# Kernel optimization log

Measured on AMD Instinct MI355X. Metric: run time of the kernel, lower is better.

## Reference

```python
import jax, jax.numpy as jnp
import numpy as np

D_MODEL = 2048
N_HEAD = 16
B, T = 2, 2048
D_HEAD = D_MODEL // N_HEAD          # 128
D_Q = D_MODEL // 3                  # 682
D_KV = D_MODEL // 2                 # 1024
D_QK_N = D_HEAD // 2                # 64
D_QK_R = D_HEAD // 2                # 64
LN_EPS = 1e-5


def setup_inputs() -> dict:
    key = jax.random.key(0)
    ks = jax.random.split(key, 8)
    s = 0.02
    return {
        'x': jax.random.normal(ks[0], (B, T, D_MODEL), dtype=jnp.float32),
        'Wdq_w': jax.random.normal(ks[1], (D_Q, D_MODEL), dtype=jnp.float32) * s,
        'Wdq_b': jnp.zeros((D_Q,), jnp.float32),
        'qn_g': jnp.ones((D_Q,), jnp.float32),
        'qn_b': jnp.zeros((D_Q,), jnp.float32),
        'Wuq_w': jax.random.normal(ks[2], (D_MODEL, D_Q), dtype=jnp.float32) * s,
        'Wuq_b': jnp.zeros((D_MODEL,), jnp.float32),
        'Wdkv_w': jax.random.normal(ks[3], (D_KV + D_QK_R, D_MODEL), dtype=jnp.float32) * s,
        'Wdkv_b': jnp.zeros((D_KV + D_QK_R,), jnp.float32),
        'kvn_g': jnp.ones((D_KV,), jnp.float32),
        'kvn_b': jnp.zeros((D_KV,), jnp.float32),
        'Wukv_w': jax.random.normal(ks[4], (D_MODEL + N_HEAD * D_QK_N, D_KV), dtype=jnp.float32) * s,
        'Wukv_b': jnp.zeros((D_MODEL + N_HEAD * D_QK_N,), jnp.float32),
        'Wo_w': jax.random.normal(ks[5], (D_MODEL, D_MODEL), dtype=jnp.float32) * s,
        'Wo_b': jnp.zeros((D_MODEL,), jnp.float32),
    }


def _linear(x, w, b):
    return jnp.einsum('...i,oi->...o', x, w) + b


def _layernorm(x, g, b):
    mu = jnp.mean(x, axis=-1, keepdims=True)
    var = jnp.mean(jnp.square(x - mu), axis=-1, keepdims=True)
    return (x - mu) * jax.lax.rsqrt(var + LN_EPS) * g + b


def _rotary(x):
    # Faithful to source: positions are taken from axis 1 of x (B, A, T, d)
    A, d = x.shape[1], x.shape[-1]
    inv_freq = (1.0 / 10000.0) ** (jnp.arange(0, d, 2, dtype=jnp.float32) / d)
    freqs = jnp.arange(A, dtype=jnp.float32)[:, None] * inv_freq[None, :]
    cos = jnp.cos(freqs)[None, :, None, :]
    sin = jnp.sin(freqs)[None, :, None, :]
    x1, x2 = jnp.split(x, 2, axis=-1)
    return jnp.concatenate([x1 * cos + x2 * sin, -x1 * sin + x2 * cos], axis=-1)


def reference(x, Wdq_w, Wdq_b, qn_g, qn_b, Wuq_w, Wuq_b,
              Wdkv_w, Wdkv_b, kvn_g, kvn_b, Wukv_w, Wukv_b, Wo_w, Wo_b):
    Bx, Tx, C = x.shape
    # Q path: down-proj -> norm -> up-proj
    c_q = _layernorm(_linear(x, Wdq_w, Wdq_b), qn_g, qn_b)
    q = _linear(c_q, Wuq_w, Wuq_b).reshape(Bx, Tx, N_HEAD, D_HEAD).transpose(0, 2, 1, 3)
    q_n, q_r = q[..., :D_QK_N], q[..., D_QK_N:]
    q_r = _rotary(q_r)
    # KV path
    c_kv = _linear(x, Wdkv_w, Wdkv_b)
    kv_n, k_r = c_kv[..., :D_KV], c_kv[..., D_KV:]
    kv_n = _layernorm(kv_n, kvn_g, kvn_b)
    kv = _linear(kv_n, Wukv_w, Wukv_b).reshape(Bx, Tx, N_HEAD, D_HEAD + D_QK_N).transpose(0, 2, 1, 3)
    k_n, v = kv[..., :D_QK_N], kv[..., D_QK_N:]
    k_r = k_r.reshape(Bx, Tx, 1, D_QK_R).transpose(0, 2, 1, 3)  # (B,1,T,dr)
    k_r = _rotary(k_r)  # identity here (single position), kept for fidelity
    k_r = jnp.broadcast_to(k_r, (Bx, N_HEAD, Tx, D_QK_R))
    q_full = jnp.concatenate([q_n, q_r], axis=-1)   # (B,H,T,d_head)
    k_full = jnp.concatenate([k_n, k_r], axis=-1)   # (B,H,T,d_head)
    # causal SDPA (scale = 1/sqrt(q dim))
    scale = 1.0 / np.sqrt(D_HEAD)
    scores = jnp.einsum('bhqd,bhkd->bhqk', q_full, k_full) * scale
    causal = jnp.tril(jnp.ones((Tx, Tx), dtype=bool))
    scores = jnp.where(causal[None, None], scores, jnp.finfo(scores.dtype).min)
    p = jax.nn.softmax(scores, axis=-1)
    y = jnp.einsum('bhqk,bhkd->bhqd', p, v)
    y = y.transpose(0, 2, 1, 3).reshape(Bx, Tx, C)
    return _linear(y, Wo_w, Wo_b)
```

## Files before the change

kernel.cpp:

```cpp
#include <hip/hip_runtime.h>
#include <math.h>

#define TOK 4096
#define DM 2048
#define DQ 682
#define DQP 704
#define DKV 1024
#define DUKV 3072
#define NH 16
#define T_SEQ 2048
#define NQKV 1792

typedef __attribute__((ext_vector_type(8))) short short8;
typedef __attribute__((ext_vector_type(4))) float floatx4;
typedef __attribute__((ext_vector_type(2))) unsigned int uint2v;

__device__ __forceinline__ unsigned short f2bf(float f) {
  union { float f; unsigned int u; } v; v.f = f;
  unsigned int u = v.u;
  u += 0x7fffu + ((u >> 16) & 1u);
  return (unsigned short)(u >> 16);
}
__device__ __forceinline__ unsigned short f2bf_fast(float f) {
  union { float f; unsigned int u; } v; v.f = f;
  return (unsigned short)((v.u + 0x8000u) >> 16);
}

typedef __attribute__((address_space(1))) const unsigned int as1_u32;
typedef __attribute__((address_space(3))) unsigned int as3_u32;
__device__ __forceinline__ void async16(const void* g, void* l) {
  __builtin_amdgcn_global_load_lds((as1_u32*)g, (as3_u32*)l, 16, 0, 0);
}

__global__ __launch_bounds__(256) void gemm_dqkv_sk(
    const unsigned short* __restrict__ A,
    const unsigned short* __restrict__ B,
    float* __restrict__ P0, float* __restrict__ P1)
{
  __shared__ __align__(16) unsigned short sm[16384];
  const int kz = blockIdx.z;
  const unsigned short* Ab = A + kz * 1024;
  const unsigned short* Bb = B + kz * 1024;
  float* C = kz ? P1 : P0;
  const int K = 1024;

  const int tid = threadIdx.x;
  const int w = tid >> 6, lane = tid & 63, q = lane >> 4, r = lane & 15;
  const int bm = blockIdx.y * 128, bn = blockIdx.x * 128;

  floatx4 acc[4][4];
#pragma unroll
  for (int i = 0; i < 4; i++)
#pragma unroll
    for (int j = 0; j < 4; j++) acc[i][j] = (floatx4){0.f, 0.f, 0.f, 0.f};

  const int srow = tid >> 2, scol = (tid & 3) * 8;
  const unsigned short* Ag0 = Ab + (size_t)(bm + srow) * 2048 + scol;
  const unsigned short* Ag1 = Ab + (size_t)(bm + 64 + srow) * 2048 + scol;
  const unsigned short* Bg0 = Bb + (size_t)(bn + srow) * 2048 + scol;
  const unsigned short* Bg1 = Bb + (size_t)(bn + 64 + srow) * 2048 + scol;
  const int mrow0 = (w >> 1) * 64, ncol0 = (w & 1) * 64;

  async16(Ag0, &sm[w * 512]);
  async16(Ag1, &sm[2048 + w * 512]);
  async16(Bg0, &sm[8192 + w * 512]);
  async16(Bg1, &sm[8192 + 2048 + w * 512]);

  for (int k0 = 0; k0 < K; k0 += 32) {
    const int cur = (k0 >> 5) & 1;
    __syncthreads();
    if (k0 + 32 < K) {
      const int nxt = cur ^ 1;
      async16(Ag0 + k0 + 32, &sm[nxt * 4096 + w * 512]);
      async16(Ag1 + k0 + 32, &sm[nxt * 4096 + 2048 + w * 512]);
      async16(Bg0 + k0 + 32, &sm[8192 + nxt * 4096 + w * 512]);
      async16(Bg1 + k0 + 32, &sm[8192 + nxt * 4096 + 2048 + w * 512]);
    }
    const unsigned short* As = &sm[cur * 4096];
    const unsigned short* Bs = &sm[8192 + cur * 4096];
    short8 a[4], b[4];
#pragma unroll
    for (int i = 0; i < 4; i++)
      a[i] = *(const short8*)&As[(mrow0 + i * 16 + r) * 32 + q * 8];
#pragma unroll
    for (int j = 0; j < 4; j++)
      b[j] = *(const short8*)&Bs[(ncol0 + j * 16 + r) * 32 + q * 8];
#pragma unroll
    for (int i = 0; i < 4; i++)
#pragma unroll
      for (int j = 0; j < 4; j++)
        acc[i][j] = __builtin_amdgcn_mfma_f32_16x16x32_bf16(a[i], b[j], acc[i][j], 0, 0, 0);
  }

#pragma unroll
  for (int j = 0; j < 4; j++) {
    int gc = bn + ncol0 + j * 16 + r;
#pragma unroll
    for (int i = 0; i < 4; i++) {
#pragma unroll
      for (int v = 0; v < 4; v++) {
        int gr = bm + mrow0 + i * 16 + q * 4 + v;
        C[(size_t)gr * NQKV + gc] = acc[i][j][v];
      }
    }
  }
}

__global__ __launch_bounds__(256) void gemm_wo64(
    const unsigned short* __restrict__ A,
    const unsigned short* __restrict__ B,
    const float* __restrict__ bias, float* __restrict__ C)
{
  __shared__ __align__(16) unsigned short sm[32768];
  const int tid = threadIdx.x;
  const int w = tid >> 6, lane = tid & 63, q = lane >> 4, r = lane & 15;
  const int bm = blockIdx.y * 128, bn = blockIdx.x * 128;

  floatx4 acc[4][4];
#pragma unroll
  for (int i = 0; i < 4; i++)
#pragma unroll
    for (int j = 0; j < 4; j++) acc[i][j] = (floatx4){0.f, 0.f, 0.f, 0.f};

  const int srow = tid >> 2, scol = (tid & 3) * 8;
  const unsigned short* Ag0 = A + (size_t)(bm + srow) * 2048 + scol;
  const unsigned short* Ag1 = A + (size_t)(bm + 64 + srow) * 2048 + scol;
  const unsigned short* Bg0 = B + (size_t)(bn + srow) * 2048 + scol;
  const unsigned short* Bg1 = B + (size_t)(bn + 64 + srow) * 2048 + scol;
  const int mrow0 = (w >> 1) * 64, ncol0 = (w & 1) * 64;

#pragma unroll
  for (int c2 = 0; c2 < 2; c2++) {
    async16(Ag0 + c2 * 32, &sm[c2 * 4096 + w * 512]);
    async16(Ag1 + c2 * 32, &sm[c2 * 4096 + 2048 + w * 512]);
    async16(Bg0 + c2 * 32, &sm[16384 + c2 * 4096 + w * 512]);
    async16(Bg1 + c2 * 32, &sm[16384 + c2 * 4096 + 2048 + w * 512]);
  }

  for (int k0 = 0; k0 < 2048; k0 += 64) {
    const int cur = (k0 >> 6) & 1;
    __syncthreads();
    if (k0 + 64 < 2048) {
      const int nxt = cur ^ 1;
#pragma unroll
      for (int c2 = 0; c2 < 2; c2++) {
        async16(Ag0 + k0 + 64 + c2 * 32, &sm[nxt * 8192 + c2 * 4096 + w * 512]);
        async16(Ag1 + k0 + 64 + c2 * 32, &sm[nxt * 8192 + c2 * 4096 + 2048 + w * 512]);
        async16(Bg0 + k0 + 64 + c2 * 32, &sm[16384 + nxt * 8192 + c2 * 4096 + w * 512]);
        async16(Bg1 + k0 + 64 + c2 * 32, &sm[16384 + nxt * 8192 + c2 * 4096 + 2048 + w * 512]);
      }
    }
#pragma unroll
    for (int c2 = 0; c2 < 2; c2++) {
      const unsigned short* As = &sm[cur * 8192 + c2 * 4096];
      const unsigned short* Bs = &sm[16384 + cur * 8192 + c2 * 4096];
      short8 a[4], b[4];
#pragma unroll
      for (int i = 0; i < 4; i++)
        a[i] = *(const short8*)&As[(mrow0 + i * 16 + r) * 32 + q * 8];
#pragma unroll
      for (int j = 0; j < 4; j++)
        b[j] = *(const short8*)&Bs[(ncol0 + j * 16 + r) * 32 + q * 8];
#pragma unroll
      for (int i = 0; i < 4; i++)
#pragma unroll
        for (int j = 0; j < 4; j++)
          acc[i][j] = __builtin_amdgcn_mfma_f32_16x16x32_bf16(a[i], b[j], acc[i][j], 0, 0, 0);
    }
  }

#pragma unroll
  for (int j = 0; j < 4; j++) {
    int gc = bn + ncol0 + j * 16 + r;
    float bv = bias[gc];
#pragma unroll
    for (int i = 0; i < 4; i++) {
#pragma unroll
      for (int v = 0; v < 4; v++) {
        int gr = bm + mrow0 + i * 16 + q * 4 + v;
        C[(size_t)gr * 2048 + gc] = acc[i][j][v] + bv;
      }
    }
  }
}

__global__ __launch_bounds__(256) void gemm_up_fused(
    const unsigned short* __restrict__ Aq, const unsigned short* __restrict__ Bq,
    const float* __restrict__ biasq, unsigned short* __restrict__ Qall,
    const unsigned short* __restrict__ Akv, const unsigned short* __restrict__ Bkv,
    const float* __restrict__ biaskv,
    unsigned short* __restrict__ Kn, unsigned short* __restrict__ Vb)
{
  __shared__ __align__(16) unsigned short sm[16384];
  const int tid = threadIdx.x;
  const int w = tid >> 6, lane = tid & 63, q = lane >> 4, r = lane & 15;
  const int bx = blockIdx.x;
  const bool isQ = bx < 16;
  const int bn = isQ ? bx * 128 : (bx - 16) * 128;
  const int bm = blockIdx.y * 128;
  const int K = isQ ? DQP : DKV;
  const unsigned short* A = isQ ? Aq : Akv;
  const unsigned short* B = isQ ? Bq : Bkv;

  floatx4 acc[4][4];
#pragma unroll
  for (int i = 0; i < 4; i++)
#pragma unroll
    for (int j = 0; j < 4; j++) acc[i][j] = (floatx4){0.f, 0.f, 0.f, 0.f};

  const int srow = tid >> 2, scol = (tid & 3) * 8;
  const unsigned short* Ag0 = A + (size_t)(bm + srow) * K + scol;
  const unsigned short* Ag1 = A + (size_t)(bm + 64 + srow) * K + scol;
  const unsigned short* Bg0 = B + (size_t)(bn + srow) * K + scol;
  const unsigned short* Bg1 = B + (size_t)(bn + 64 + srow) * K + scol;
  const int mrow0 = (w >> 1) * 64, ncol0 = (w & 1) * 64;

  async16(Ag0, &sm[w * 512]);
  async16(Ag1, &sm[2048 + w * 512]);
  async16(Bg0, &sm[8192 + w * 512]);
  async16(Bg1, &sm[8192 + 2048 + w * 512]);

  for (int k0 = 0; k0 < K; k0 += 32) {
    const int cur = (k0 >> 5) & 1;
    __syncthreads();
    if (k0 + 32 < K) {
      const int nxt = cur ^ 1;
      async16(Ag0 + k0 + 32, &sm[nxt * 4096 + w * 512]);
      async16(Ag1 + k0 + 32, &sm[nxt * 4096 + 2048 + w * 512]);
      async16(Bg0 + k0 + 32, &sm[8192 + nxt * 4096 + w * 512]);
      async16(Bg1 + k0 + 32, &sm[8192 + nxt * 4096 + 2048 + w * 512]);
    }
    const unsigned short* As = &sm[cur * 4096];
    const unsigned short* Bs = &sm[8192 + cur * 4096];
    short8 a[4], b[4];
#pragma unroll
    for (int i = 0; i < 4; i++)
      a[i] = *(const short8*)&As[(mrow0 + i * 16 + r) * 32 + q * 8];
#pragma unroll
    for (int j = 0; j < 4; j++)
      b[j] = *(const short8*)&Bs[(ncol0 + j * 16 + r) * 32 + q * 8];
#pragma unroll
    for (int i = 0; i < 4; i++)
#pragma unroll
      for (int j = 0; j < 4; j++)
        acc[i][j] = __builtin_amdgcn_mfma_f32_16x16x32_bf16(a[i], b[j], acc[i][j], 0, 0, 0);
  }

  if (!isQ) {
#pragma unroll
    for (int j = 0; j < 4; j++) {
      int gc = bn + ncol0 + j * 16 + r;
      float bv = biaskv[gc];
      int hh = gc / 192;
      int rel = gc - hh * 192;
#pragma unroll
      for (int i = 0; i < 4; i++) {
#pragma unroll
        for (int v = 0; v < 4; v++) {
          int gr = bm + mrow0 + i * 16 + q * 4 + v;
          int bb = gr >> 11, tt = gr & 2047;
          int bhh = bb * NH + hh;
          int kt = tt >> 6;
          unsigned short val = f2bf(acc[i][j][v] + bv);
          if (rel < 64) {
            Kn[((size_t)(bhh * 32 + kt)) * 4096 + (rel >> 5) * 2048 +
               (tt & 63) * 32 + (rel & 31)] = val;
          } else {
            int d = rel - 64;
            Vb[((size_t)(bhh * 32 + kt)) * 8192 + ((tt >> 5) & 1) * 4096 +
               d * 32 + (tt & 31)] = val;
          }
        }
      }
    }
    return;
  }

  const int h = bx;
  const float QS = (float)(0.08838834764831845 * 1.4426950408889634);
  if ((w & 1) == 0) {
#pragma unroll
    for (int j = 0; j < 4; j++) {
      int d = j * 16 + r;
      float bv = biasq[h * 128 + d];
#pragma unroll
      for (int i = 0; i < 4; i++) {
#pragma unroll
        for (int v = 0; v < 4; v++) {
          int gr = bm + mrow0 + i * 16 + q * 4 + v;
          int bb = gr >> 11, t = gr & 2047;
          Qall[(((size_t)(bb * NH + h)) * T_SEQ + t) * 128 + d] =
              f2bf((acc[i][j][v] + bv) * QS);
        }
      }
    }
  } else {
    float cs[2], sn[2], bv1[2], bv2[2];
#pragma unroll
    for (int jp = 0; jp < 2; jp++) {
      int jj = jp * 16 + r;
      float ang = (float)h * exp2f(-(float)jj * (13.287712379549449f / 32.0f));
      cs[jp] = cosf(ang); sn[jp] = sinf(ang);
      bv1[jp] = biasq[h * 128 + 64 + jj];
      bv2[jp] = biasq[h * 128 + 96 + jj];
    }
#pragma unroll
    for (int i = 0; i < 4; i++) {
#pragma unroll
      for (int v = 0; v < 4; v++) {
        int gr = bm + mrow0 + i * 16 + q * 4 + v;
        int bb = gr >> 11, t = gr & 2047;
        unsigned short* Qr = Qall + (((size_t)(bb * NH + h)) * T_SEQ + t) * 128;
#pragma unroll
        for (int jp = 0; jp < 2; jp++) {
          int jj = jp * 16 + r;
          float x1 = acc[i][jp][v] + bv1[jp];
          float x2 = acc[i][jp + 2][v] + bv2[jp];
          Qr[64 + jj] = f2bf((x1 * cs[jp] + x2 * sn[jp]) * QS);
          Qr[96 + jj] = f2bf((x2 * cs[jp] - x1 * sn[jp]) * QS);
        }
      }
    }
  }
}

__device__ __forceinline__ void cvt_region(
    const float* __restrict__ in, unsigned short* __restrict__ out,
    int irows, int icols, int ocols, long idx)
{
  int rr = (int)(idx / ocols);
  int cc = (int)(idx - (long)rr * ocols);
  out[idx] = (rr < irows && cc < icols) ? f2bf(in[(size_t)rr * icols + cc]) : 0;
}

__global__ __launch_bounds__(256) void prep_all(
    const float* __restrict__ x,
    const float* __restrict__ Wdq_w, const float* __restrict__ Wdkv_w,
    const float* __restrict__ Wuq_w, const float* __restrict__ Wukv_w,
    const float* __restrict__ Wo_w,
    const float* __restrict__ Wdq_b, const float* __restrict__ Wdkv_b,
    unsigned short* __restrict__ x_bf,
    unsigned short* __restrict__ Wqkv_bf, unsigned short* __restrict__ Wuq_bf,
    unsigned short* __restrict__ Wukv_bf, unsigned short* __restrict__ Wo_bf,
    float* __restrict__ bias_qkv)
{
  const long bx = blockIdx.x;
  if (bx < 32768) {
    long idx = bx * 256 + threadIdx.x;
    x_bf[idx] = f2bf(x[idx]);
  } else if (bx < 38400) {
    cvt_region(Wdq_w, Wqkv_bf, 682, 2048, 2048, (bx - 32768) * 256 + threadIdx.x);
  } else if (bx < 47104) {
    cvt_region(Wdkv_w, Wqkv_bf + 704L * 2048, 1088, 2048, 2048,
               (bx - 38400) * 256 + threadIdx.x);
  } else if (bx < 52736) {
    cvt_region(Wuq_w, Wuq_bf, 2048, 682, 704, (bx - 47104) * 256 + threadIdx.x);
  } else if (bx < 65024) {
    cvt_region(Wukv_w, Wukv_bf, 3072, 1024, 1024, (bx - 52736) * 256 + threadIdx.x);
  } else if (bx < 81408) {
    cvt_region(Wo_w, Wo_bf, 2048, 2048, 2048, (bx - 65024) * 256 + threadIdx.x);
  } else {
    int i = (int)(bx - 81408) * 256 + threadIdx.x;
    if (i < NQKV)
      bias_qkv[i] = (i < DQ) ? Wdq_b[i] : ((i < DQP) ? 0.f : Wdkv_b[i - DQP]);
  }
}

__global__ __launch_bounds__(256) void ln_dual_r(
    const float* __restrict__ p0, const float* __restrict__ p1,
    const float* __restrict__ bqkv,
    unsigned short* __restrict__ outq, unsigned short* __restrict__ outkv,
    unsigned short* __restrict__ Kr,
    const float* __restrict__ qg, const float* __restrict__ qb2,
    const float* __restrict__ kg, const float* __restrict__ kb2)
{
  __shared__ float sbuf[8];
  const int blk = blockIdx.x;
  if (blk >= 8192) {
    const int base = (blk - 8192) * 512;
#pragma unroll
    for (int s = 0; s < 2; s++) {
      int idx = base + s * 256 + threadIdx.x;
      int row = idx >> 6, dr = idx & 63;
      size_t off = (size_t)row * NQKV + 1728 + dr;
      float v = p0[off] + p1[off] + bqkv[1728 + dr];
      Kr[((size_t)((row >> 11) * 32 + ((row & 2047) >> 6))) * 4096 +
         (dr >> 5) * 2048 + (row & 63) * 32 + (dr & 31)] = f2bf(v);
    }
    return;
  }
  const bool isQ = blk < 4096;
  const int r2 = isQ ? blk : blk - 4096;
  const int off = isQ ? 0 : DQP;
  const float* x0 = p0 + (size_t)r2 * NQKV + off;
  const float* x1 = p1 + (size_t)r2 * NQKV + off;
  const float* bb = bqkv + off;
  const int D = isQ ? DQ : DKV;
  const int ocols = isQ ? DQP : DKV;
  const float* g = isQ ? qg : kg;
  const float* bta = isQ ? qb2 : kb2;
  unsigned short* orow = (isQ ? outq : outkv) + (size_t)r2 * ocols;

  float s = 0.f, s2 = 0.f;
  for (int i = threadIdx.x; i < D; i += 256) {
    float v = x0[i] + x1[i] + bb[i];
    s += v; s2 += v * v;
  }
#pragma unroll
  for (int o = 32; o > 0; o >>= 1) {
    s += __shfl_down(s, o, 64);
    s2 += __shfl_down(s2, o, 64);
  }
  int wid = threadIdx.x >> 6;
  __syncthreads();
  if ((threadIdx.x & 63) == 0) { sbuf[wid] = s; sbuf[4 + wid] = s2; }
  __syncthreads();
  float su = sbuf[0] + sbuf[1] + sbuf[2] + sbuf[3];
  float sq = sbuf[4] + sbuf[5] + sbuf[6] + sbuf[7];
  float mu = su / (float)D;
  float var = sq / (float)D - mu * mu;
  float rstd = rsqrtf(var + 1e-5f);
  for (int i = threadIdx.x; i < ocols; i += 256) {
    float v = (i < D) ? ((x0[i] + x1[i] + bb[i]) - mu) * rstd * g[i] + bta[i] : 0.f;
    orow[i] = (i < D) ? f2bf(v) : 0;
  }
}

__global__ __launch_bounds__(256, 2) void attn_mfma5(
    const unsigned short* __restrict__ Qall,
    const unsigned short* __restrict__ Kn,
    const unsigned short* __restrict__ Kr,
    const unsigned short* __restrict__ Vb,
    unsigned short* __restrict__ y)
{
  __shared__ __align__(16) unsigned short sm[37376];
  const int id = (int)blockIdx.x;
  const int bhid = id & 31;
  const int pr = id >> 5;
  const int h = bhid & 15, b = bhid >> 4;
  const int tid = threadIdx.x;
  const int w = tid >> 6, lane = tid & 63, q = lane >> 4, r = lane & 15;
  const int bh = bhid;

  const char* KnG = (const char*)(Kn + (size_t)bh * 32 * 4096);
  const char* KrG = (const char*)(Kr + (size_t)b * 32 * 4096);
  const char* VG  = (const char*)(Vb + (size_t)bh * 32 * 8192);
  char* smB = (char*)sm;
  unsigned short* Psw = sm + 32768 + w * 1152;

#define PREFETCH_KV(kt_, buf_)                                                 \
  {                                                                            \
    const char* kn_ = KnG + (size_t)(kt_) * 8192;                              \
    const char* kr_ = KrG + (size_t)(kt_) * 8192;                              \
    const char* vg_ = VG + (size_t)(kt_) * 16384;                              \
    char* kd_ = smB + (buf_) * 16384;                                          \
    char* vd_ = smB + 32768 + (buf_) * 16384;                                  \
    _Pragma("unroll")                                                          \
    for (int i_ = 0; i_ < 2; i_++) {                                           \
      async16(kn_ + i_ * 4096 + w * 1024 + lane * 16,                          \
              kd_ + i_ * 4096 + w * 1024);                                     \
      async16(kr_ + i_ * 4096 + w * 1024 + lane * 16,                          \
              kd_ + 8192 + i_ * 4096 + w * 1024);                              \
    }                                                                          \
    _Pragma("unroll")                                                          \
    for (int i_ = 0; i_ < 4; i_++)                                             \
      async16(vg_ + i_ * 4096 + w * 1024 + lane * 16,                          \
              vd_ + i_ * 4096 + w * 1024);                                     \
  }

  for (int seg = 0; seg < 2; seg++) {
    const int a = seg ? (31 - pr) : pr;
    if (seg) __syncthreads();
    PREFETCH_KV(0, 0);

    short8 qb[4];
    const unsigned short* Qrow =
        Qall + ((size_t)bh * T_SEQ + (size_t)a * 64 + w * 16 + r) * 128 + q * 8;
#pragma unroll
    for (int c = 0; c < 4; c++) qb[c] = *(const short8*)(Qrow + c * 32);

    floatx4 oacc[8];
#pragma unroll
    for (int jd = 0; jd < 8; jd++) oacc[jd] = (floatx4){0.f, 0.f, 0.f, 0.f};
    float m_i = -3.0e38f, l_i = 0.f;

    for (int kt = 0; kt <= a; kt++) {
      const int cur = kt & 1;
      __syncthreads();
      if (kt < a) PREFETCH_KV(kt + 1, cur ^ 1);

      const unsigned short* KsC = sm + cur * 8192;
      const unsigned short* VsC = sm + 16384 + cur * 8192;

      floatx4 sacc[4];
#pragma unroll
      for (int j = 0; j < 4; j++) sacc[j] = (floatx4){0.f, 0.f, 0.f, 0.f};
#pragma unroll
      for (int c = 0; c < 4; c++) {
        short8 ak[4];
#pragma unroll
        for (int j = 0; j < 4; j++)
          ak[j] = *(const short8*)&KsC[c * 2048 + (j * 16 + r) * 32 + q * 8];
#pragma unroll
        for (int j = 0; j < 4; j++)
          sacc[j] = __builtin_amdgcn_mfma_f32_16x16x32_bf16(ak[j], qb[c], sacc[j], 0, 0, 0);
      }

      float sv[16];
#pragma unroll
      for (int j = 0; j < 4; j++)
#pragma unroll
        for (int v = 0; v < 4; v++) sv[j * 4 + v] = sacc[j][v];
      const int rel = (a - kt) * 64 + w * 16 + r;
      if (rel < 63) {
#pragma unroll
        for (int j = 0; j < 4; j++)
#pragma unroll
          for (int v = 0; v < 4; v++)
            if (j * 16 + q * 4 + v > rel) sv[j * 4 + v] = -3.0e38f;
      }
      float rm = sv[0];
#pragma unroll
      for (int t16 = 1; t16 < 16; t16++) rm = fmaxf(rm, sv[t16]);
      rm = fmaxf(rm, __shfl_xor(rm, 16, 64));
      rm = fmaxf(rm, __shfl_xor(rm, 32, 64));
      float mnew = fmaxf(m_i, rm);
      float alpha = exp2f(m_i - mnew);
      m_i = mnew;
      float p[16], rsum = 0.f;
#pragma unroll
      for (int t16 = 0; t16 < 16; t16++) { p[t16] = exp2f(sv[t16] - mnew); rsum += p[t16]; }
      rsum += __shfl_xor(rsum, 16, 64);
      rsum += __shfl_xor(rsum, 32, 64);
      l_i = l_i * alpha + rsum;
#pragma unroll
      for (int jd = 0; jd < 8; jd++) {
        oacc[jd][0] *= alpha; oacc[jd][1] *= alpha;
        oacc[jd][2] *= alpha; oacc[jd][3] *= alpha;
      }
#pragma unroll
      for (int j = 0; j < 4; j++) {
        unsigned int lo = (unsigned int)f2bf_fast(p[j * 4 + 0]) |
                          ((unsigned int)f2bf_fast(p[j * 4 + 1]) << 16);
        unsigned int hi = (unsigned int)f2bf_fast(p[j * 4 + 2]) |
                          ((unsigned int)f2bf_fast(p[j * 4 + 3]) << 16);
        uint2v pk; pk[0] = lo; pk[1] = hi;
        *(uint2v*)&Psw[r * 72 + j * 16 + q * 4] = pk;
      }
#pragma unroll
      for (int c2 = 0; c2 < 2; c2++) {
        short8 pb = *(const short8*)&Psw[r * 72 + c2 * 32 + q * 8];
#pragma unroll
        for (int jd = 0; jd < 8; jd++) {
          short8 bv = *(const short8*)&VsC[c2 * 4096 + (jd * 16 + r) * 32 + q * 8];
          oacc[jd] = __builtin_amdgcn_mfma_f32_16x16x32_bf16(bv, pb, oacc[jd], 0, 0, 0);
        }
      }
    }

    float inv = 1.0f / l_i;
    unsigned short* yr =
        y + ((size_t)(b * T_SEQ) + (size_t)a * 64 + w * 16 + r) * DM + h * 128;
#pragma unroll
    for (int jd = 0; jd < 8; jd++) {
      unsigned short o0 = f2bf(oacc[jd][0] * inv);
      unsigned short o1 = f2bf(oacc[jd][1] * inv);
      unsigned short o2 = f2bf(oacc[jd][2] * inv);
      unsigned short o3 = f2bf(oacc[jd][3] * inv);
      unsigned int lo = (unsigned int)o0 | ((unsigned int)o1 << 16);
      unsigned int hi = (unsigned int)o2 | ((unsigned int)o3 << 16);
      unsigned int* dst = (unsigned int*)(yr + jd * 16 + q * 4);
      dst[0] = lo; dst[1] = hi;
    }
  }
#undef PREFETCH_KV
}

extern "C" void kernel_launch(void* const* d_in, const int* in_sizes, int n_in,
                              void* d_out, int out_size, void* d_ws, size_t ws_size,
                              hipStream_t stream) {
  const float* x      = (const float*)d_in[0];
  const float* Wdq_w  = (const float*)d_in[1];
  const float* Wdq_b  = (const float*)d_in[2];
  const float* qn_g   = (const float*)d_in[3];
  const float* qn_b   = (const float*)d_in[4];
  const float* Wuq_w  = (const float*)d_in[5];
  const float* Wuq_b  = (const float*)d_in[6];
  const float* Wdkv_w = (const float*)d_in[7];
  const float* Wdkv_b = (const float*)d_in[8];
  const float* kvn_g  = (const float*)d_in[9];
  const float* kvn_b  = (const float*)d_in[10];
  const float* Wukv_w = (const float*)d_in[11];
  const float* Wukv_b = (const float*)d_in[12];
  const float* Wo_w   = (const float*)d_in[13];
  const float* Wo_b   = (const float*)d_in[14];
  float* out = (float*)d_out;

  float* ws = (float*)d_ws;
  unsigned short* x_bf    = (unsigned short*)(ws);
  unsigned short* y_bf    = (unsigned short*)(ws);
  unsigned short* Wqkv_bf = (unsigned short*)(ws + 4194304);
  unsigned short* Wuq_bf  = (unsigned short*)(ws + 6029312);
  unsigned short* Wukv_bf = (unsigned short*)(ws + 6750208);
  float* bias_qkv = ws + 8323072;
  float* p0       = ws + 8324864;
  float* p1       = ws + 15664896;
  unsigned short* c_q_bf = (unsigned short*)(ws + 23004928);
  unsigned short* kvn_bf = (unsigned short*)(ws + 24446720);
  unsigned short* Q_all  = (unsigned short*)(ws + 26543872);
  unsigned short* Kn_blk = (unsigned short*)(ws + 30738176);
  unsigned short* Kr_blk = (unsigned short*)(ws + 32835328);
  unsigned short* V_blk  = (unsigned short*)(ws + 32966400);
  unsigned short* Wo_bf  = (unsigned short*)(ws + 37160704);

  dim3 blk(256);

  prep_all<<<81415, blk, 0, stream>>>(x, Wdq_w, Wdkv_w, Wuq_w, Wukv_w, Wo_w,
                                      Wdq_b, Wdkv_b,
                                      x_bf, Wqkv_bf, Wuq_bf, Wukv_bf, Wo_bf,
                                      bias_qkv);
  gemm_dqkv_sk<<<dim3(14, 32, 2), blk, 0, stream>>>(x_bf, Wqkv_bf, p0, p1);
  ln_dual_r<<<8704, blk, 0, stream>>>(p0, p1, bias_qkv, c_q_bf, kvn_bf, Kr_blk,
                                      qn_g, qn_b, kvn_g, kvn_b);
  gemm_up_fused<<<dim3(40, 32), blk, 0, stream>>>(c_q_bf, Wuq_bf, Wuq_b, Q_all,
                                                  kvn_bf, Wukv_bf, Wukv_b,
                                                  Kn_blk, V_blk);
  attn_mfma5<<<512, blk, 0, stream>>>(Q_all, Kn_blk, Kr_blk, V_blk, y_bf);
  gemm_wo64<<<dim3(16, 32), blk, 0, stream>>>(y_bf, Wo_bf, Wo_b, out);
}
```

Baseline: 413.8 us.

## Swizzle K/V shared layouts, lazily rescale softmax, prioritize MFMA, cache LN values

Producers of the Kn, Kr and V blocks now store them with an XOR swizzle on the inner 32-element chunk, and the attention kernel reads with a matching swizzled offset. This is meant to cut LDS bank conflicts on the K and V fragment loads. The online softmax now rescales the accumulators only when some lane's new row max exceeds the running max by more than 8 (in log2 units), skipping most alpha multiplies. It also uses tree reductions for the max and sum, and raises wave priority around the MFMA loops. The layernorm kernel keeps its loaded values in registers so it does not reread the inputs for the output pass. Lazy rescaling lets the exponentials grow up to 2^8 before a rescale, which trades some numerical headroom for fewer multiplies.

```diff
diff --git a/kernel.cpp b/kernel.cpp
--- a/kernel.cpp
+++ b/kernel.cpp
@@ -264,11 +264,11 @@
           unsigned short val = f2bf(acc[i][j][v] + bv);
           if (rel < 64) {
             Kn[((size_t)(bhh * 32 + kt)) * 4096 + (rel >> 5) * 2048 +
-               (tt & 63) * 32 + (rel & 31)] = val;
+               (tt & 63) * 32 + ((rel & 31) ^ (((tt >> 1) & 3) << 3))] = val;
           } else {
             int d = rel - 64;
             Vb[((size_t)(bhh * 32 + kt)) * 8192 + ((tt >> 5) & 1) * 4096 +
-               d * 32 + (tt & 31)] = val;
+               d * 32 + ((tt & 31) ^ (((d >> 1) & 3) << 3))] = val;
           }
         }
       }
@@ -385,7 +385,8 @@
       size_t off = (size_t)row * NQKV + 1728 + dr;
       float v = p0[off] + p1[off] + bqkv[1728 + dr];
       Kr[((size_t)((row >> 11) * 32 + ((row & 2047) >> 6))) * 4096 +
-         (dr >> 5) * 2048 + (row & 63) * 32 + (dr & 31)] = f2bf(v);
+         (dr >> 5) * 2048 + (row & 63) * 32 +
+         ((dr & 31) ^ (((row >> 1) & 3) << 3))] = f2bf(v);
     }
     return;
   }
@@ -402,9 +403,15 @@
   unsigned short* orow = (isQ ? outq : outkv) + (size_t)r2 * ocols;
 
   float s = 0.f, s2 = 0.f;
-  for (int i = threadIdx.x; i < D; i += 256) {
-    float v = x0[i] + x1[i] + bb[i];
-    s += v; s2 += v * v;
+  float vv[4];
+#pragma unroll
+  for (int ii = 0; ii < 4; ii++) {
+    int i = threadIdx.x + ii * 256;
+    if (i < D) {
+      float v = x0[i] + x1[i] + bb[i];
+      vv[ii] = v;
+      s += v; s2 += v * v;
+    }
   }
 #pragma unroll
   for (int o = 32; o > 0; o >>= 1) {
@@ -420,13 +427,15 @@
   float mu = su / (float)D;
   float var = sq / (float)D - mu * mu;
   float rstd = rsqrtf(var + 1e-5f);
-  for (int i = threadIdx.x; i < ocols; i += 256) {
-    float v = (i < D) ? ((x0[i] + x1[i] + bb[i]) - mu) * rstd * g[i] + bta[i] : 0.f;
-    orow[i] = (i < D) ? f2bf(v) : 0;
-  }
-}
-
-__global__ __launch_bounds__(256, 2) void attn_mfma5(
+#pragma unroll
+  for (int ii = 0; ii < 4; ii++) {
+    int i = threadIdx.x + ii * 256;
+    if (i < ocols)
+      orow[i] = (i < D) ? f2bf((vv[ii] - mu) * rstd * g[i] + bta[i]) : 0;
+  }
+}
+
+__global__ __launch_bounds__(256, 2) void attn_mfma6(
     const unsigned short* __restrict__ Qall,
     const unsigned short* __restrict__ Kn,
     const unsigned short* __restrict__ Kr,
@@ -441,6 +450,7 @@
   const int tid = threadIdx.x;
   const int w = tid >> 6, lane = tid & 63, q = lane >> 4, r = lane & 15;
   const int bh = bhid;
+  const int sq8 = (q ^ ((r >> 1) & 3)) * 8;
 
   const char* KnG = (const char*)(Kn + (size_t)bh * 32 * 4096);
   const char* KrG = (const char*)(Kr + (size_t)b * 32 * 4096);
@@ -495,16 +505,18 @@
       floatx4 sacc[4];
 #pragma unroll
       for (int j = 0; j < 4; j++) sacc[j] = (floatx4){0.f, 0.f, 0.f, 0.f};
+      __builtin_amdgcn_s_setprio(1);
 #pragma unroll
       for (int c = 0; c < 4; c++) {
         short8 ak[4];
 #pragma unroll
         for (int j = 0; j < 4; j++)
-          ak[j] = *(const short8*)&KsC[c * 2048 + (j * 16 + r) * 32 + q * 8];
+          ak[j] = *(const short8*)&KsC[c * 2048 + (j * 16 + r) * 32 + sq8];
 #pragma unroll
         for (int j = 0; j < 4; j++)
           sacc[j] = __builtin_amdgcn_mfma_f32_16x16x32_bf16(ak[j], qb[c], sacc[j], 0, 0, 0);
       }
+      __builtin_amdgcn_s_setprio(0);
 
       float sv[16];
 #pragma unroll
@@ -519,25 +531,37 @@
           for (int v = 0; v < 4; v++)
             if (j * 16 + q * 4 + v > rel) sv[j * 4 + v] = -3.0e38f;
       }
-      float rm = sv[0];
-#pragma unroll
-      for (int t16 = 1; t16 < 16; t16++) rm = fmaxf(rm, sv[t16]);
+      float tm[8];
+#pragma unroll
+      for (int t = 0; t < 8; t++) tm[t] = fmaxf(sv[t], sv[t + 8]);
+#pragma unroll
+      for (int t = 0; t < 4; t++) tm[t] = fmaxf(tm[t], tm[t + 4]);
+      float rm = fmaxf(fmaxf(tm[0], tm[2]), fmaxf(tm[1], tm[3]));
       rm = fmaxf(rm, __shfl_xor(rm, 16, 64));
       rm = fmaxf(rm, __shfl_xor(rm, 32, 64));
-      float mnew = fmaxf(m_i, rm);
-      float alpha = exp2f(m_i - mnew);
-      m_i = mnew;
-      float p[16], rsum = 0.f;
-#pragma unroll
-      for (int t16 = 0; t16 < 16; t16++) { p[t16] = exp2f(sv[t16] - mnew); rsum += p[t16]; }
+      if (__any(rm > m_i + 8.f)) {
+        float mnew = fmaxf(m_i, rm);
+        float alpha = exp2f(m_i - mnew);
+        m_i = mnew;
+        l_i *= alpha;
+#pragma unroll
+        for (int jd = 0; jd < 8; jd++) {
+          oacc[jd][0] *= alpha; oacc[jd][1] *= alpha;
+          oacc[jd][2] *= alpha; oacc[jd][3] *= alpha;
+        }
+      }
+      float p[16];
+#pragma unroll
+      for (int t = 0; t < 16; t++) p[t] = exp2f(sv[t] - m_i);
+      float ts[8];
+#pragma unroll
+      for (int t = 0; t < 8; t++) ts[t] = p[t] + p[t + 8];
+#pragma unroll
+      for (int t = 0; t < 4; t++) ts[t] = ts[t] + ts[t + 4];
+      float rsum = (ts[0] + ts[2]) + (ts[1] + ts[3]);
       rsum += __shfl_xor(rsum, 16, 64);
       rsum += __shfl_xor(rsum, 32, 64);
-      l_i = l_i * alpha + rsum;
-#pragma unroll
-      for (int jd = 0; jd < 8; jd++) {
-        oacc[jd][0] *= alpha; oacc[jd][1] *= alpha;
-        oacc[jd][2] *= alpha; oacc[jd][3] *= alpha;
-      }
+      l_i += rsum;
 #pragma unroll
       for (int j = 0; j < 4; j++) {
         unsigned int lo = (unsigned int)f2bf_fast(p[j * 4 + 0]) |
@@ -547,15 +571,17 @@
         uint2v pk; pk[0] = lo; pk[1] = hi;
         *(uint2v*)&Psw[r * 72 + j * 16 + q * 4] = pk;
       }
+      __builtin_amdgcn_s_setprio(1);
 #pragma unroll
       for (int c2 = 0; c2 < 2; c2++) {
         short8 pb = *(const short8*)&Psw[r * 72 + c2 * 32 + q * 8];
 #pragma unroll
         for (int jd = 0; jd < 8; jd++) {
-          short8 bv = *(const short8*)&VsC[c2 * 4096 + (jd * 16 + r) * 32 + q * 8];
+          short8 bv = *(const short8*)&VsC[c2 * 4096 + (jd * 16 + r) * 32 + sq8];
           oacc[jd] = __builtin_amdgcn_mfma_f32_16x16x32_bf16(bv, pb, oacc[jd], 0, 0, 0);
         }
       }
+      __builtin_amdgcn_s_setprio(0);
     }
 
     float inv = 1.0f / l_i;
@@ -625,6 +651,6 @@
   gemm_up_fused<<<dim3(40, 32), blk, 0, stream>>>(c_q_bf, Wuq_bf, Wuq_b, Q_all,
                                                   kvn_bf, Wukv_bf, Wukv_b,
                                                   Kn_blk, V_blk);
-  attn_mfma5<<<512, blk, 0, stream>>>(Q_all, Kn_blk, Kr_blk, V_blk, y_bf);
+  attn_mfma6<<<512, blk, 0, stream>>>(Q_all, Kn_blk, Kr_blk, V_blk, y_bf);
   gemm_wo64<<<dim3(16, 32), blk, 0, stream>>>(y_bf, Wo_bf, Wo_b, out);
 }
```

New measurement: 396.1 us. -4.3%, faster.
